# Performance work log

Hardware: AMD Instinct MI355X
Metric: run time of the kernel (lower is better)

Reference implementation:

```python
import jax, jax.numpy as jnp
import numpy as np

N_NODES = 100000
N_EDGES = 1600000
F_IN = 512
HID = 128
N_CLASS = 6


def setup_inputs() -> dict:
    key = jax.random.key(0)
    ks = jax.random.split(key, 12)
    def unif(k, shape, stdv):
        return jax.random.uniform(k, shape, jnp.float32, -stdv, stdv)
    s1 = 1.0 / np.sqrt(HID); s4 = 1.0 / np.sqrt(N_CLASS)
    return {
        "x": jax.random.normal(ks[0], (N_NODES, F_IN), jnp.float32),
        "edge_row": jax.random.randint(ks[1], (N_EDGES,), 0, N_NODES, jnp.int32),
        "edge_col": jax.random.randint(ks[2], (N_EDGES,), 0, N_NODES, jnp.int32),
        "edge_weight": jax.random.uniform(ks[3], (N_EDGES,), jnp.float32),
        "W1": unif(ks[4], (F_IN, HID), s1), "b1": unif(ks[5], (HID,), s1),
        "W2": unif(ks[6], (HID, HID), s1), "b2": unif(ks[7], (HID,), s1),
        "W3": unif(ks[8], (HID, HID), s1), "b3": unif(ks[9], (HID,), s1),
        "W4": unif(ks[10], (HID, N_CLASS), s4), "b4": unif(ks[11], (N_CLASS,), s4),
    }


def _gcn_layer(x, row, col, w_e, W, b):
    # support = x @ W  (dense mm), then spmm(adj, support) in COO form:
    # out[i] = sum_{(i,j) in E} A[i,j] * support[j]
    support = x @ W                              # [N, F_out]
    msgs = support[col] * w_e[:, None]           # [E, F_out] gather + scale
    agg = jax.ops.segment_sum(msgs, row, num_segments=N_NODES)
    return agg + b


def reference(x, edge_row, edge_col, edge_weight, W1, b1, W2, b2, W3, b3, W4, b4):
    # eval mode: F.dropout(training=False) is identity
    h = jax.nn.relu(_gcn_layer(x, edge_row, edge_col, edge_weight, W1, b1))
    h = jax.nn.relu(_gcn_layer(h, edge_row, edge_col, edge_weight, W2, b2))
    h = jax.nn.relu(_gcn_layer(h, edge_row, edge_col, edge_weight, W3, b3))
    return _gcn_layer(h, edge_row, edge_col, edge_weight, W4, b4)
```

## Files before the change

### kernel.cpp

```cpp
#include <hip/hip_runtime.h>
#include <cstdint>

constexpr int NN = 100000;
constexpr int NE = 1600000;
constexpr int FIN = 512;
constexpr int HID = 128;
constexpr int NCLS = 6;
constexpr int EPAD = NE + 7 * NN;

typedef __attribute__((ext_vector_type(8))) short short8v;
typedef __attribute__((ext_vector_type(4))) float f32x4;

__device__ __forceinline__ unsigned short f2bf(float f) {
    uint32_t u = __float_as_uint(f);
    uint32_t r = u + 0x7FFFu + ((u >> 16) & 1u);
    return (unsigned short)(r >> 16);
}
__device__ __forceinline__ float bflo(uint32_t u) { return __uint_as_float(u << 16); }
__device__ __forceinline__ float bfhi(uint32_t u) { return __uint_as_float(u & 0xffff0000u); }

__device__ __forceinline__ void gl_lds16(const void* g, void* l) {
    __builtin_amdgcn_global_load_lds(
        (const __attribute__((address_space(1))) unsigned int*)(unsigned long long)g,
        (__attribute__((address_space(3))) unsigned int*)(unsigned int)(unsigned long long)l,
        16, 0, 0);
}

__global__ void cvt_w(const float* __restrict__ W, unsigned short* __restrict__ Bp, int K) {
    const int t = blockIdx.x * blockDim.x + threadIdx.x;
    const int total = (K / 32) * 8 * 64;
    if (t >= total) return;
    const int lane = t & 63;
    const int fi = t >> 6;
    const int n = fi & 7, ks = fi >> 3;
    const int krow = ks * 32 + (lane >> 4) * 8;
    const int col = n * 16 + (lane & 15);
    short8v sv;
    #pragma unroll
    for (int j = 0; j < 8; ++j) sv[j] = (short)f2bf(W[(size_t)(krow + j) * HID + col]);
    *(short8v*)&Bp[(size_t)t * 8] = sv;
}

template<int K, bool ABF>
__launch_bounds__(320)
__global__ void gemm_lds(const void* __restrict__ Av, const unsigned short* __restrict__ Bp,
                         unsigned short* __restrict__ C) {
    constexpr int BM    = 160;
    constexpr int KS    = 32;
    constexpr int EB    = ABF ? 2 : 4;
    constexpr int ROWB  = KS * EB;
    constexpr int SLOTS = ROWB / 16;
    constexpr int SMSK  = SLOTS - 1;
    constexpr int CHUNK = BM * ROWB;
    constexpr int WBYT  = CHUNK / 5;
    constexpr int NISS  = WBYT / 1024;
    constexpr int NS    = K / KS;

    __shared__ __attribute__((aligned(16))) unsigned char lds[2 * CHUNK];

    const int tid  = threadIdx.x;
    const int lane = tid & 63;
    const int wave = tid >> 6;
    const int row0 = blockIdx.x * BM;
    const int lr   = lane & 15;
    const int kg   = lane >> 4;

    const unsigned char* Ab = (const unsigned char*)Av;
    const size_t rowbytes = (size_t)K * EB;

    auto stage = [&](int bufsel, int ks) {
        const size_t kbyte = (size_t)ks * ROWB;
        #pragma unroll
        for (int i = 0; i < NISS; ++i) {
            const int Lw   = wave * WBYT + i * 1024 + lane * 16;
            const int row  = Lw / ROWB;
            const int slot = (Lw >> 4) & SMSK;
            const int src  = slot ^ (row & SMSK);
            const unsigned char* g = Ab + (size_t)(row0 + row) * rowbytes + kbyte + src * 16;
            void* l = (void*)&lds[bufsel * CHUNK + wave * WBYT + i * 1024];
            gl_lds16(g, l);
        }
    };

    f32x4 acc[2][8] = {};

    stage(0, 0);
    __syncthreads();

    int cur = 0;
    for (int ks = 0; ks < NS; ++ks) {
        if (ks + 1 < NS) stage(cur ^ 1, ks + 1);

        const unsigned char* base = &lds[cur * CHUNK];
        const int rA0 = wave * 32 + lr;
        const int rA1 = rA0 + 16;
        const int key = lr & SMSK;

        short8v a0, a1;
        if constexpr (ABF) {
            a0 = *(const short8v*)(base + rA0 * ROWB + ((kg ^ key) * 16));
            a1 = *(const short8v*)(base + rA1 * ROWB + ((kg ^ key) * 16));
        } else {
            const float4 f00 = *(const float4*)(base + rA0 * ROWB + (((2 * kg + 0) ^ key) * 16));
            const float4 f01 = *(const float4*)(base + rA0 * ROWB + (((2 * kg + 1) ^ key) * 16));
            const float4 f10 = *(const float4*)(base + rA1 * ROWB + (((2 * kg + 0) ^ key) * 16));
            const float4 f11 = *(const float4*)(base + rA1 * ROWB + (((2 * kg + 1) ^ key) * 16));
            a0[0] = (short)f2bf(f00.x); a0[1] = (short)f2bf(f00.y);
            a0[2] = (short)f2bf(f00.z); a0[3] = (short)f2bf(f00.w);
            a0[4] = (short)f2bf(f01.x); a0[5] = (short)f2bf(f01.y);
            a0[6] = (short)f2bf(f01.z); a0[7] = (short)f2bf(f01.w);
            a1[0] = (short)f2bf(f10.x); a1[1] = (short)f2bf(f10.y);
            a1[2] = (short)f2bf(f10.z); a1[3] = (short)f2bf(f10.w);
            a1[4] = (short)f2bf(f11.x); a1[5] = (short)f2bf(f11.y);
            a1[6] = (short)f2bf(f11.z); a1[7] = (short)f2bf(f11.w);
        }

        const unsigned short* bb = Bp + ((size_t)ks * 8 * 64 + lane) * 8;
        #pragma unroll
        for (int n = 0; n < 8; ++n) {
            const short8v b = *reinterpret_cast<const short8v*>(bb + (size_t)n * 64 * 8);
            acc[0][n] = __builtin_amdgcn_mfma_f32_16x16x32_bf16(a0, b, acc[0][n], 0, 0, 0);
            acc[1][n] = __builtin_amdgcn_mfma_f32_16x16x32_bf16(a1, b, acc[1][n], 0, 0, 0);
        }
        __syncthreads();
        cur ^= 1;
    }

    #pragma unroll
    for (int m = 0; m < 2; ++m)
        #pragma unroll
        for (int n = 0; n < 8; ++n)
            #pragma unroll
            for (int i = 0; i < 4; ++i) {
                const int r = row0 + wave * 32 + m * 16 + kg * 4 + i;
                C[(size_t)r * HID + n * 16 + lr] = f2bf(acc[m][n][i]);
            }
}

__global__ void gemm_w4(const unsigned short* __restrict__ H, const float* __restrict__ W,
                        float* __restrict__ S, int M) {
    __shared__ float Ws[HID * NCLS];
    for (int i = threadIdx.x; i < HID * NCLS; i += blockDim.x) Ws[i] = W[i];
    __syncthreads();
    const int r = blockIdx.x * blockDim.x + threadIdx.x;
    if (r >= M) return;
    float acc[NCLS] = {};
    const unsigned short* h = &H[(size_t)r * HID];
    for (int k0 = 0; k0 < HID; k0 += 8) {
        const uint4 hv = *reinterpret_cast<const uint4*>(&h[k0]);
        float hf[8];
        hf[0] = bflo(hv.x); hf[1] = bfhi(hv.x);
        hf[2] = bflo(hv.y); hf[3] = bfhi(hv.y);
        hf[4] = bflo(hv.z); hf[5] = bfhi(hv.z);
        hf[6] = bflo(hv.w); hf[7] = bfhi(hv.w);
        #pragma unroll
        for (int u = 0; u < 8; ++u)
            #pragma unroll
            for (int j = 0; j < NCLS; ++j)
                acc[j] = fmaf(hf[u], Ws[(k0 + u) * NCLS + j], acc[j]);
    }
    #pragma unroll
    for (int j = 0; j < NCLS; ++j) S[(size_t)r * NCLS + j] = acc[j];
}

__global__ void hist_k(const int* __restrict__ erow, int* __restrict__ cnt) {
    const int e = blockIdx.x * blockDim.x + threadIdx.x;
    if (e < NE) atomicAdd(&cnt[erow[e]], 1);
}

__global__ void scan1_k(const int* __restrict__ in, int* __restrict__ out,
                        int* __restrict__ bsum, int n) {
    __shared__ int s[256];
    const int tid = threadIdx.x;
    const int gid = blockIdx.x * 256 + tid;
    const int v = (gid < NN) ? ((in[gid] + 7) & ~7) : 0;
    s[tid] = v;
    __syncthreads();
    for (int off = 1; off < 256; off <<= 1) {
        const int t = (tid >= off) ? s[tid - off] : 0;
        __syncthreads();
        s[tid] += t;
        __syncthreads();
    }
    if (gid < n) out[gid] = s[tid] - v;
    if (tid == 255) bsum[blockIdx.x] = s[255];
}

__global__ void scan2_k(int* __restrict__ bsum, int nb) {
    __shared__ int s[512];
    const int tid = threadIdx.x;
    const int v = (tid < nb) ? bsum[tid] : 0;
    s[tid] = v;
    __syncthreads();
    for (int off = 1; off < 512; off <<= 1) {
        const int t = (tid >= off) ? s[tid - off] : 0;
        __syncthreads();
        s[tid] += t;
        __syncthreads();
    }
    if (tid < nb) bsum[tid] = s[tid] - v;
}

__global__ void scan3_k(int* __restrict__ out, const int* __restrict__ bsum, int n) {
    const int gid = blockIdx.x * 256 + threadIdx.x;
    if (gid < n) out[gid] += bsum[blockIdx.x];
}

__global__ void scatter_k(const int* __restrict__ erow, const int* __restrict__ ecol,
                          const float* __restrict__ ew,
                          const int* __restrict__ row_ptr, int* __restrict__ cur,
                          int2* __restrict__ edges) {
    const int e = blockIdx.x * blockDim.x + threadIdx.x;
    if (e >= NE) return;
    const int r = erow[e];
    const int pos = row_ptr[r] + atomicAdd(&cur[r], 1);
    edges[pos] = make_int2(ecol[e], __float_as_int(ew[e]));
}

template<bool RELU>
__launch_bounds__(256)
__global__ void spmm_bf16(const int* __restrict__ row_ptr,
                          const int2* __restrict__ edges,
                          const unsigned short* __restrict__ S,
                          const float* __restrict__ bias,
                          unsigned short* __restrict__ out) {
    const int lane = threadIdx.x & 63;
    const int row = blockIdx.x * 4 + (threadIdx.x >> 6);
    if (row >= NN) return;
    const int beg = row_ptr[row];
    const int end = row_ptr[row + 1];
    const int fo = lane * 2;
    float2 a0 = *reinterpret_cast<const float2*>(&bias[fo]);
    float2 a1 = {0.f, 0.f}, a2 = {0.f, 0.f}, a3 = {0.f, 0.f};

    for (int j = beg; j < end; j += 8) {
        const int4 p0 = *reinterpret_cast<const int4*>(edges + j);
        const int4 p1 = *reinterpret_cast<const int4*>(edges + j + 2);
        const int4 p2 = *reinterpret_cast<const int4*>(edges + j + 4);
        const int4 p3 = *reinterpret_cast<const int4*>(edges + j + 6);
        const uint32_t s0 = *reinterpret_cast<const uint32_t*>(&S[(size_t)p0.x * HID + fo]);
        const uint32_t s1 = *reinterpret_cast<const uint32_t*>(&S[(size_t)p0.z * HID + fo]);
        const uint32_t s2 = *reinterpret_cast<const uint32_t*>(&S[(size_t)p1.x * HID + fo]);
        const uint32_t s3 = *reinterpret_cast<const uint32_t*>(&S[(size_t)p1.z * HID + fo]);
        const uint32_t s4 = *reinterpret_cast<const uint32_t*>(&S[(size_t)p2.x * HID + fo]);
        const uint32_t s5 = *reinterpret_cast<const uint32_t*>(&S[(size_t)p2.z * HID + fo]);
        const uint32_t s6 = *reinterpret_cast<const uint32_t*>(&S[(size_t)p3.x * HID + fo]);
        const uint32_t s7 = *reinterpret_cast<const uint32_t*>(&S[(size_t)p3.z * HID + fo]);
        const float w0 = __int_as_float(p0.y), w1 = __int_as_float(p0.w);
        const float w2 = __int_as_float(p1.y), w3 = __int_as_float(p1.w);
        const float w4 = __int_as_float(p2.y), w5 = __int_as_float(p2.w);
        const float w6 = __int_as_float(p3.y), w7 = __int_as_float(p3.w);
        a0.x = fmaf(bflo(s0), w0, a0.x); a0.y = fmaf(bfhi(s0), w0, a0.y);
        a1.x = fmaf(bflo(s1), w1, a1.x); a1.y = fmaf(bfhi(s1), w1, a1.y);
        a2.x = fmaf(bflo(s2), w2, a2.x); a2.y = fmaf(bfhi(s2), w2, a2.y);
        a3.x = fmaf(bflo(s3), w3, a3.x); a3.y = fmaf(bfhi(s3), w3, a3.y);
        a0.x = fmaf(bflo(s4), w4, a0.x); a0.y = fmaf(bfhi(s4), w4, a0.y);
        a1.x = fmaf(bflo(s5), w5, a1.x); a1.y = fmaf(bfhi(s5), w5, a1.y);
        a2.x = fmaf(bflo(s6), w6, a2.x); a2.y = fmaf(bfhi(s6), w6, a2.y);
        a3.x = fmaf(bflo(s7), w7, a3.x); a3.y = fmaf(bfhi(s7), w7, a3.y);
    }
    float fx = (a0.x + a1.x) + (a2.x + a3.x);
    float fy = (a0.y + a1.y) + (a2.y + a3.y);
    if (RELU) { fx = fmaxf(fx, 0.f); fy = fmaxf(fy, 0.f); }
    const uint32_t o = (uint32_t)f2bf(fx) | ((uint32_t)f2bf(fy) << 16);
    *reinterpret_cast<uint32_t*>(&out[(size_t)row * HID + fo]) = o;
}

__launch_bounds__(256)
__global__ void spmm6(const int* __restrict__ row_ptr,
                      const int2* __restrict__ edges,
                      const float* __restrict__ S,
                      const float* __restrict__ bias,
                      float* __restrict__ out) {
    const int t = blockIdx.x * blockDim.x + threadIdx.x;
    const int row = t >> 4;
    const int sl = t & 15;
    if (row >= NN) return;
    const int beg = row_ptr[row];
    const int end = row_ptr[row + 1];
    float acc[NCLS] = {};
    for (int j = beg + sl; j < end; j += 16) {
        const int2 e = edges[j];
        const float w = __int_as_float(e.y);
        const float* s = &S[(size_t)e.x * NCLS];
        #pragma unroll
        for (int k = 0; k < NCLS; ++k) acc[k] = fmaf(s[k], w, acc[k]);
    }
    #pragma unroll
    for (int off = 8; off > 0; off >>= 1)
        #pragma unroll
        for (int k = 0; k < NCLS; ++k) acc[k] += __shfl_xor(acc[k], off, 64);
    if (sl == 0) {
        #pragma unroll
        for (int k = 0; k < NCLS; ++k) out[(size_t)row * NCLS + k] = acc[k] + bias[k];
    }
}

extern "C" void kernel_launch(void* const* d_in, const int* in_sizes, int n_in,
                              void* d_out, int out_size, void* d_ws, size_t ws_size,
                              hipStream_t stream) {
    const float* x    = (const float*)d_in[0];
    const int*   erow = (const int*)d_in[1];
    const int*   ecol = (const int*)d_in[2];
    const float* ew   = (const float*)d_in[3];
    const float* W1 = (const float*)d_in[4];  const float* b1 = (const float*)d_in[5];
    const float* W2 = (const float*)d_in[6];  const float* b2 = (const float*)d_in[7];
    const float* W3 = (const float*)d_in[8];  const float* b3 = (const float*)d_in[9];
    const float* W4 = (const float*)d_in[10]; const float* b4 = (const float*)d_in[11];
    float* out = (float*)d_out;

    int2*           edges_s = (int2*)d_ws;
    unsigned short* sup16   = (unsigned short*)(edges_s + EPAD);
    unsigned short* h16     = sup16 + (size_t)NN * HID;
    float*          sup6    = (float*)(h16 + (size_t)NN * HID);
    unsigned short* Bp1     = (unsigned short*)(sup6 + (size_t)NN * NCLS);
    unsigned short* Bp2     = Bp1 + (size_t)FIN * HID;
    unsigned short* Bp3     = Bp2 + (size_t)HID * HID;
    int*            row_ptr = (int*)(Bp3 + (size_t)HID * HID);
    int*            row_cnt = row_ptr + (NN + 1);
    int*            bsum    = row_cnt + NN;

    const dim3 blk(256);
    const int  g_edge = (NE + 255) / 256;
    const int  NB = (NN + 1 + 255) / 256;

    cvt_w<<<(FIN / 32 * 8 * 64 + 255) / 256, blk, 0, stream>>>(W1, Bp1, FIN);
    cvt_w<<<(HID / 32 * 8 * 64 + 255) / 256, blk, 0, stream>>>(W2, Bp2, HID);
    cvt_w<<<(HID / 32 * 8 * 64 + 255) / 256, blk, 0, stream>>>(W3, Bp3, HID);

    hipMemsetAsync(row_cnt, 0, (size_t)NN * sizeof(int), stream);
    hipMemsetAsync(edges_s, 0, (size_t)EPAD * sizeof(int2), stream);
    hist_k<<<g_edge, blk, 0, stream>>>(erow, row_cnt);
    scan1_k<<<NB, blk, 0, stream>>>(row_cnt, row_ptr, bsum, NN + 1);
    scan2_k<<<1, 512, 0, stream>>>(bsum, NB);
    scan3_k<<<NB, blk, 0, stream>>>(row_ptr, bsum, NN + 1);
    hipMemsetAsync(row_cnt, 0, (size_t)NN * sizeof(int), stream);
    scatter_k<<<g_edge, blk, 0, stream>>>(erow, ecol, ew, row_ptr, row_cnt, edges_s);

    const int g_gemm = NN / 160;
    const int g_spmm = NN / 4;

    gemm_lds<FIN, false><<<g_gemm, dim3(320), 0, stream>>>(x, Bp1, sup16);
    spmm_bf16<true><<<g_spmm, blk, 0, stream>>>(row_ptr, edges_s, sup16, b1, h16);
    gemm_lds<HID, true><<<g_gemm, dim3(320), 0, stream>>>(h16, Bp2, sup16);
    spmm_bf16<true><<<g_spmm, blk, 0, stream>>>(row_ptr, edges_s, sup16, b2, h16);
    gemm_lds<HID, true><<<g_gemm, dim3(320), 0, stream>>>(h16, Bp3, sup16);
    spmm_bf16<true><<<g_spmm, blk, 0, stream>>>(row_ptr, edges_s, sup16, b3, h16);
    gemm_w4<<<(NN + 255) / 256, blk, 0, stream>>>(h16, W4, sup6, NN);
    spmm6<<<(NN * 16 + 255) / 256, blk, 0, stream>>>(row_ptr, edges_s, sup6, b4, out);
}
```

Before: 495.2 us.

## Drop GEMM block barriers, fuse weight conversion, pad edges instead of memset, unroll SpMM

```diff
diff --git a/kernel.cpp b/kernel.cpp
--- a/kernel.cpp
+++ b/kernel.cpp
@@ -26,10 +26,8 @@
         16, 0, 0);
 }
 
-__global__ void cvt_w(const float* __restrict__ W, unsigned short* __restrict__ Bp, int K) {
-    const int t = blockIdx.x * blockDim.x + threadIdx.x;
-    const int total = (K / 32) * 8 * 64;
-    if (t >= total) return;
+__device__ __forceinline__ void cvt_body(const float* __restrict__ W,
+                                         unsigned short* __restrict__ Bp, int t) {
     const int lane = t & 63;
     const int fi = t >> 6;
     const int n = fi & 7, ks = fi >> 3;
@@ -39,6 +37,18 @@
     #pragma unroll
     for (int j = 0; j < 8; ++j) sv[j] = (short)f2bf(W[(size_t)(krow + j) * HID + col]);
     *(short8v*)&Bp[(size_t)t * 8] = sv;
+}
+
+__global__ void cvt_w3(const float* __restrict__ W1, const float* __restrict__ W2,
+                       const float* __restrict__ W3,
+                       unsigned short* __restrict__ Bp1, unsigned short* __restrict__ Bp2,
+                       unsigned short* __restrict__ Bp3) {
+    const int t = blockIdx.x * blockDim.x + threadIdx.x;
+    constexpr int T1 = (FIN / 32) * 8 * 64;
+    constexpr int T2 = (HID / 32) * 8 * 64;
+    if (t < T1)                cvt_body(W1, Bp1, t);
+    else if (t < T1 + T2)      cvt_body(W2, Bp2, t - T1);
+    else if (t < T1 + 2 * T2)  cvt_body(W3, Bp3, t - T1 - T2);
 }
 
 template<int K, bool ABF>
@@ -85,11 +95,16 @@
     f32x4 acc[2][8] = {};
 
     stage(0, 0);
-    __syncthreads();
 
     int cur = 0;
     for (int ks = 0; ks < NS; ++ks) {
-        if (ks + 1 < NS) stage(cur ^ 1, ks + 1);
+        if (ks + 1 < NS) {
+            stage(cur ^ 1, ks + 1);
+            asm volatile("s_waitcnt vmcnt(%0)" :: "i"(NISS) : "memory");
+        } else {
+            asm volatile("s_waitcnt vmcnt(0)" ::: "memory");
+        }
+        __builtin_amdgcn_sched_barrier(0);
 
         const unsigned char* base = &lds[cur * CHUNK];
         const int rA0 = wave * 32 + lr;
@@ -122,7 +137,6 @@
             acc[0][n] = __builtin_amdgcn_mfma_f32_16x16x32_bf16(a0, b, acc[0][n], 0, 0, 0);
             acc[1][n] = __builtin_amdgcn_mfma_f32_16x16x32_bf16(a1, b, acc[1][n], 0, 0, 0);
         }
-        __syncthreads();
         cur ^= 1;
     }
 
@@ -217,6 +231,14 @@
     edges[pos] = make_int2(ecol[e], __float_as_int(ew[e]));
 }
 
+__global__ void pad_k(const int* __restrict__ row_ptr, const int* __restrict__ cur,
+                      int2* __restrict__ edges) {
+    const int r = blockIdx.x * blockDim.x + threadIdx.x;
+    if (r >= NN) return;
+    const int end = row_ptr[r + 1];
+    for (int p = row_ptr[r] + cur[r]; p < end; ++p) edges[p] = make_int2(0, 0);
+}
+
 template<bool RELU>
 __launch_bounds__(256)
 __global__ void spmm_bf16(const int* __restrict__ row_ptr,
@@ -233,31 +255,46 @@
     float2 a0 = *reinterpret_cast<const float2*>(&bias[fo]);
     float2 a1 = {0.f, 0.f}, a2 = {0.f, 0.f}, a3 = {0.f, 0.f};
 
-    for (int j = beg; j < end; j += 8) {
-        const int4 p0 = *reinterpret_cast<const int4*>(edges + j);
-        const int4 p1 = *reinterpret_cast<const int4*>(edges + j + 2);
-        const int4 p2 = *reinterpret_cast<const int4*>(edges + j + 4);
-        const int4 p3 = *reinterpret_cast<const int4*>(edges + j + 6);
-        const uint32_t s0 = *reinterpret_cast<const uint32_t*>(&S[(size_t)p0.x * HID + fo]);
-        const uint32_t s1 = *reinterpret_cast<const uint32_t*>(&S[(size_t)p0.z * HID + fo]);
-        const uint32_t s2 = *reinterpret_cast<const uint32_t*>(&S[(size_t)p1.x * HID + fo]);
-        const uint32_t s3 = *reinterpret_cast<const uint32_t*>(&S[(size_t)p1.z * HID + fo]);
-        const uint32_t s4 = *reinterpret_cast<const uint32_t*>(&S[(size_t)p2.x * HID + fo]);
-        const uint32_t s5 = *reinterpret_cast<const uint32_t*>(&S[(size_t)p2.z * HID + fo]);
-        const uint32_t s6 = *reinterpret_cast<const uint32_t*>(&S[(size_t)p3.x * HID + fo]);
-        const uint32_t s7 = *reinterpret_cast<const uint32_t*>(&S[(size_t)p3.z * HID + fo]);
-        const float w0 = __int_as_float(p0.y), w1 = __int_as_float(p0.w);
-        const float w2 = __int_as_float(p1.y), w3 = __int_as_float(p1.w);
-        const float w4 = __int_as_float(p2.y), w5 = __int_as_float(p2.w);
-        const float w6 = __int_as_float(p3.y), w7 = __int_as_float(p3.w);
-        a0.x = fmaf(bflo(s0), w0, a0.x); a0.y = fmaf(bfhi(s0), w0, a0.y);
-        a1.x = fmaf(bflo(s1), w1, a1.x); a1.y = fmaf(bfhi(s1), w1, a1.y);
-        a2.x = fmaf(bflo(s2), w2, a2.x); a2.y = fmaf(bfhi(s2), w2, a2.y);
-        a3.x = fmaf(bflo(s3), w3, a3.x); a3.y = fmaf(bfhi(s3), w3, a3.y);
-        a0.x = fmaf(bflo(s4), w4, a0.x); a0.y = fmaf(bfhi(s4), w4, a0.y);
-        a1.x = fmaf(bflo(s5), w5, a1.x); a1.y = fmaf(bfhi(s5), w5, a1.y);
-        a2.x = fmaf(bflo(s6), w6, a2.x); a2.y = fmaf(bfhi(s6), w6, a2.y);
-        a3.x = fmaf(bflo(s7), w7, a3.x); a3.y = fmaf(bfhi(s7), w7, a3.y);
+    int j = beg;
+    for (; j + 16 <= end; j += 16) {
+        int4 p[8];
+        #pragma unroll
+        for (int q = 0; q < 8; ++q) p[q] = *reinterpret_cast<const int4*>(edges + j + 2 * q);
+        uint32_t s[16];
+        #pragma unroll
+        for (int q = 0; q < 8; ++q) {
+            s[2 * q]     = *reinterpret_cast<const uint32_t*>(&S[(size_t)p[q].x * HID + fo]);
+            s[2 * q + 1] = *reinterpret_cast<const uint32_t*>(&S[(size_t)p[q].z * HID + fo]);
+        }
+        #pragma unroll
+        for (int q = 0; q < 4; ++q) {
+            const float w0 = __int_as_float(p[q].y), w1 = __int_as_float(p[q].w);
+            const float w2 = __int_as_float(p[q + 4].y), w3 = __int_as_float(p[q + 4].w);
+            a0.x = fmaf(bflo(s[2*q]),   w0, a0.x); a0.y = fmaf(bfhi(s[2*q]),   w0, a0.y);
+            a1.x = fmaf(bflo(s[2*q+1]), w1, a1.x); a1.y = fmaf(bfhi(s[2*q+1]), w1, a1.y);
+            a2.x = fmaf(bflo(s[2*q+8]), w2, a2.x); a2.y = fmaf(bfhi(s[2*q+8]), w2, a2.y);
+            a3.x = fmaf(bflo(s[2*q+9]), w3, a3.x); a3.y = fmaf(bfhi(s[2*q+9]), w3, a3.y);
+        }
+    }
+    for (; j < end; j += 8) {
+        int4 p[4];
+        #pragma unroll
+        for (int q = 0; q < 4; ++q) p[q] = *reinterpret_cast<const int4*>(edges + j + 2 * q);
+        uint32_t s[8];
+        #pragma unroll
+        for (int q = 0; q < 4; ++q) {
+            s[2 * q]     = *reinterpret_cast<const uint32_t*>(&S[(size_t)p[q].x * HID + fo]);
+            s[2 * q + 1] = *reinterpret_cast<const uint32_t*>(&S[(size_t)p[q].z * HID + fo]);
+        }
+        #pragma unroll
+        for (int q = 0; q < 2; ++q) {
+            const float w0 = __int_as_float(p[q].y), w1 = __int_as_float(p[q].w);
+            const float w2 = __int_as_float(p[q + 2].y), w3 = __int_as_float(p[q + 2].w);
+            a0.x = fmaf(bflo(s[2*q]),   w0, a0.x); a0.y = fmaf(bfhi(s[2*q]),   w0, a0.y);
+            a1.x = fmaf(bflo(s[2*q+1]), w1, a1.x); a1.y = fmaf(bfhi(s[2*q+1]), w1, a1.y);
+            a2.x = fmaf(bflo(s[2*q+4]), w2, a2.x); a2.y = fmaf(bfhi(s[2*q+4]), w2, a2.y);
+            a3.x = fmaf(bflo(s[2*q+5]), w3, a3.x); a3.y = fmaf(bfhi(s[2*q+5]), w3, a3.y);
+        }
     }
     float fx = (a0.x + a1.x) + (a2.x + a3.x);
     float fy = (a0.y + a1.y) + (a2.y + a3.y);
@@ -318,24 +355,22 @@
     unsigned short* Bp3     = Bp2 + (size_t)HID * HID;
     int*            row_ptr = (int*)(Bp3 + (size_t)HID * HID);
     int*            row_cnt = row_ptr + (NN + 1);
-    int*            bsum    = row_cnt + NN;
+    int*            row_cur = row_cnt + NN;
+    int*            bsum    = row_cur + NN;
 
     const dim3 blk(256);
     const int  g_edge = (NE + 255) / 256;
     const int  NB = (NN + 1 + 255) / 256;
 
-    cvt_w<<<(FIN / 32 * 8 * 64 + 255) / 256, blk, 0, stream>>>(W1, Bp1, FIN);
-    cvt_w<<<(HID / 32 * 8 * 64 + 255) / 256, blk, 0, stream>>>(W2, Bp2, HID);
-    cvt_w<<<(HID / 32 * 8 * 64 + 255) / 256, blk, 0, stream>>>(W3, Bp3, HID);
-
-    hipMemsetAsync(row_cnt, 0, (size_t)NN * sizeof(int), stream);
-    hipMemsetAsync(edges_s, 0, (size_t)EPAD * sizeof(int2), stream);
+    cvt_w3<<<(12288 + 255) / 256, blk, 0, stream>>>(W1, W2, W3, Bp1, Bp2, Bp3);
+
+    hipMemsetAsync(row_cnt, 0, (size_t)2 * NN * sizeof(int), stream);
     hist_k<<<g_edge, blk, 0, stream>>>(erow, row_cnt);
     scan1_k<<<NB, blk, 0, stream>>>(row_cnt, row_ptr, bsum, NN + 1);
     scan2_k<<<1, 512, 0, stream>>>(bsum, NB);
     scan3_k<<<NB, blk, 0, stream>>>(row_ptr, bsum, NN + 1);
-    hipMemsetAsync(row_cnt, 0, (size_t)NN * sizeof(int), stream);
-    scatter_k<<<g_edge, blk, 0, stream>>>(erow, ecol, ew, row_ptr, row_cnt, edges_s);
+    scatter_k<<<g_edge, blk, 0, stream>>>(erow, ecol, ew, row_ptr, row_cur, edges_s);
+    pad_k<<<(NN + 255) / 256, blk, 0, stream>>>(row_ptr, row_cur, edges_s);
 
     const int g_gemm = NN / 160;
     const int g_spmm = NN / 4;
```

After: 483.7 us. 2.3% less time.
